# Kernel tuning notes

Hardware: AMD Instinct MI355X
Metric: run time of the kernel (lower is better)

The kernel has to match this reference:

```python
import jax, jax.numpy as jnp
import numpy as np

B, T, C = 4, 2048, 1024
WIN = 16


def setup_inputs() -> dict:
    key = jax.random.key(0)
    ks = jax.random.split(key, 5)
    s = 1.0 / np.sqrt(C)
    return {
        "x": jax.random.normal(ks[0], (B, T, C), dtype=jnp.float32),
        "Wq": jax.random.normal(ks[1], (C, C), dtype=jnp.float32) * s,
        "bq": jnp.zeros((C,), jnp.float32),
        "Wk": jax.random.normal(ks[2], (C, C), dtype=jnp.float32) * s,
        "bk": jnp.zeros((C,), jnp.float32),
        "Wv": jax.random.normal(ks[3], (C, C), dtype=jnp.float32) * s,
        "bv": jnp.zeros((C,), jnp.float32),
        "Wo": jax.random.normal(ks[4], (C, C), dtype=jnp.float32) * s,
        "bo": jnp.zeros((C,), jnp.float32),
        "window": WIN,
    }


def reference(x, Wq, bq, Wk, bk, Wv, bv, Wo, bo, window):
    Bn, Tn, Cn = x.shape
    half = window // 2
    W = 2 * half + 1  # keys per query (window [t-half, t+half])
    q = x @ Wq.T + bq
    k = x @ Wk.T + bk
    v = x @ Wv.T + bv
    offs = jnp.arange(-half, half + 1)              # [W]
    tpos = jnp.arange(Tn)                            # [T]
    idx = tpos[:, None] + offs[None, :]              # [T, W]
    valid = (idx >= 0) & (idx < Tn)                  # [T, W]
    idx_c = jnp.clip(idx, 0, Tn - 1)
    k_win = k[:, idx_c, :]                           # [B, T, W, C]
    v_win = v[:, idx_c, :]                           # [B, T, W, C]
    scale = 1.0 / jnp.sqrt(jnp.asarray(Cn, x.dtype))
    scores = jnp.einsum('btc,btwc->btw', q, k_win) * scale
    scores = jnp.where(valid[None, :, :], scores, jnp.finfo(x.dtype).min)
    attn = jax.nn.softmax(scores, axis=-1)           # [B, T, W]
    ctx = jnp.einsum('btw,btwc->btc', attn, v_win)   # [B, T, C]
    return ctx @ Wo.T + bo
```

## Files before the change

kernel.cpp:

```cpp
#include <hip/hip_runtime.h>
#include <cstdint>
#include <cstddef>

#define B_ 4
#define T_ 2048
#define C_ 1024
#define M_ (B_ * T_)
#define HALF_ 8
#define W_ 17
#define QKV_STRIDE 3072
#define NT 32
#define ATOK 16

typedef unsigned short u16;
typedef _Float16 half8 __attribute__((ext_vector_type(8)));
typedef _Float16 half2_t __attribute__((ext_vector_type(2)));
typedef float f32x16 __attribute__((ext_vector_type(16)));
typedef unsigned short ushort8v __attribute__((ext_vector_type(8)));

__device__ __forceinline__ float dot16(half8 a, half8 b, float acc) {
#if __has_builtin(__builtin_amdgcn_fdot2)
    const half2_t* pa = (const half2_t*)&a;
    const half2_t* pb = (const half2_t*)&b;
#pragma unroll
    for (int e = 0; e < 4; ++e) acc = __builtin_amdgcn_fdot2(pa[e], pb[e], acc, false);
#else
#pragma unroll
    for (int e = 0; e < 8; ++e) acc += (float)a[e] * (float)b[e];
#endif
    return acc;
}

__device__ __forceinline__ ushort4 cvt4(float4 v) {
    ushort4 o;
    _Float16 a = (_Float16)v.x; o.x = __builtin_bit_cast(unsigned short, a);
    _Float16 b = (_Float16)v.y; o.y = __builtin_bit_cast(unsigned short, b);
    _Float16 c = (_Float16)v.z; o.z = __builtin_bit_cast(unsigned short, c);
    _Float16 d = (_Float16)v.w; o.w = __builtin_bit_cast(unsigned short, d);
    return o;
}


__global__ void prologue2(const float* __restrict__ x,
                          const float* __restrict__ Wq, const float* __restrict__ Wk,
                          const float* __restrict__ Wv, const float* __restrict__ Wo,
                          const float* __restrict__ bq, const float* __restrict__ bk,
                          const float* __restrict__ bv,
                          u16* __restrict__ xf, u16* __restrict__ wfq,
                          u16* __restrict__ wfo, float* __restrict__ bcat) {
    const int blk = blockIdx.x;
    const int tid = threadIdx.x;
    if (blk >= 3072) {
        int i = (blk - 3072) * 256 + tid;
        const float* src = (i < 1024) ? bq : (i < 2048) ? bk : bv;
        bcat[i] = src[i & 1023];
        return;
    }
    __shared__ ushort8v g16[512];
    const float* src;
    u16* dst;
    size_t chunk_base;
    int kg;
    if (blk < 2048) {
        const int mt = blk >> 3; kg = blk & 7;
        src = x + (size_t)mt * 32 * C_;
        dst = xf; chunk_base = (size_t)mt * 64;
    } else {
        const int w = blk - 2048;
        const int mat = w >> 8, nt = (w >> 3) & 31; kg = w & 7;
        src = ((mat == 0) ? Wq : (mat == 1) ? Wk : (mat == 2) ? Wv : Wo)
              + (size_t)nt * 32 * C_;
        if (mat < 3) { dst = wfq; chunk_base = (size_t)(mat * 32 + nt) * 64; }
        else         { dst = wfo; chunk_base = (size_t)nt * 64; }
    }
    const int r = tid >> 3, gc = (tid & 7) * 2;
    const float4* s4 = (const float4*)(src + (size_t)r * C_ + kg * 128 + (tid & 7) * 16);
    float4 f0 = s4[0], f1 = s4[1], f2 = s4[2], f3 = s4[3];
    ushort4 h0 = cvt4(f0), h1 = cvt4(f1), h2 = cvt4(f2), h3 = cvt4(f3);
    ushort8v ga, gb;
    ga[0]=h0.x; ga[1]=h0.y; ga[2]=h0.z; ga[3]=h0.w;
    ga[4]=h1.x; ga[5]=h1.y; ga[6]=h1.z; ga[7]=h1.w;
    gb[0]=h2.x; gb[1]=h2.y; gb[2]=h2.z; gb[3]=h2.w;
    gb[4]=h3.x; gb[5]=h3.y; gb[6]=h3.z; gb[7]=h3.w;
    g16[r * 16 + ((gc    ) ^ (r & 15))] = ga;
    g16[r * 16 + ((gc + 1) ^ (r & 15))] = gb;
    __syncthreads();
    const int lane = tid & 63, rr = lane & 31, hi = lane >> 5;
#pragma unroll
    for (int r2 = 0; r2 < 2; ++r2) {
        const int ksl = r2 * 4 + (tid >> 6);
        const int g = ksl * 2 + hi;
        ushort8v v = g16[rr * 16 + (g ^ (rr & 15))];
        *(ushort8v*)(dst + ((chunk_base + kg * 8 + ksl) * 64 + lane) * 8) = v;
    }
}


#define AS1_ __attribute__((address_space(1)))
#define AS3_ __attribute__((address_space(3)))

__device__ __forceinline__ void gload16(const u16* g, u16* l) {
    __builtin_amdgcn_global_load_lds((AS1_ void*)g, (AS3_ void*)l, 16, 0, 0);
}

#define MFMA_ __builtin_amdgcn_mfma_f32_32x32x16_f16

#define STAGE(NB, KT) { const size_t ko = (size_t)(KT) * 1024;            \
    gload16(gA0 + ko, (NB) + lA0); gload16(gA1 + ko, (NB) + lA1);         \
    gload16(gA2 + ko, (NB) + lA2); gload16(gA3 + ko, (NB) + lA3);         \
    gload16(gB0 + ko, (NB) + lB0); gload16(gB1 + ko, (NB) + lB1); }

#define TILE(CB, NB, KT, DOSTG, VW)                                        \
  {                                                                        \
    half8 a0 = *(const half8*)((CB) + oA);                                 \
    half8 a1 = *(const half8*)((CB) + oA + 1024);                          \
    half8 a2 = *(const half8*)((CB) + oA + 2048);                          \
    half8 a3 = *(const half8*)((CB) + oA + 3072);                          \
    half8 b0v = *(const half8*)((CB) + oB);                                \
    half8 b1v = *(const half8*)((CB) + oB + 1024);                         \
    if (DOSTG) STAGE(NB, (KT) + 2);                                        \
    __builtin_amdgcn_s_setprio(1);                                         \
    acc00 = MFMA_(a0, b0v, acc00, 0, 0, 0);                                \
    acc01 = MFMA_(a0, b1v, acc01, 0, 0, 0);                                \
    acc10 = MFMA_(a1, b0v, acc10, 0, 0, 0);                                \
    acc11 = MFMA_(a1, b1v, acc11, 0, 0, 0);                                \
    acc20 = MFMA_(a2, b0v, acc20, 0, 0, 0);                                \
    acc21 = MFMA_(a2, b1v, acc21, 0, 0, 0);                                \
    acc30 = MFMA_(a3, b0v, acc30, 0, 0, 0);                                \
    acc31 = MFMA_(a3, b1v, acc31, 0, 0, 0);                                \
    __builtin_amdgcn_s_setprio(0);                                         \
    a0 = *(const half8*)((CB) + oA + 512);                                 \
    a1 = *(const half8*)((CB) + oA + 1536);                                \
    a2 = *(const half8*)((CB) + oA + 2560);                                \
    a3 = *(const half8*)((CB) + oA + 3584);                                \
    b0v = *(const half8*)((CB) + oB + 512);                                \
    b1v = *(const half8*)((CB) + oB + 1536);                               \
    __builtin_amdgcn_s_setprio(1);                                         \
    acc00 = MFMA_(a0, b0v, acc00, 0, 0, 0);                                \
    acc01 = MFMA_(a0, b1v, acc01, 0, 0, 0);                                \
    acc10 = MFMA_(a1, b0v, acc10, 0, 0, 0);                                \
    acc11 = MFMA_(a1, b1v, acc11, 0, 0, 0);                                \
    acc20 = MFMA_(a2, b0v, acc20, 0, 0, 0);                                \
    acc21 = MFMA_(a2, b1v, acc21, 0, 0, 0);                                \
    acc30 = MFMA_(a3, b0v, acc30, 0, 0, 0);                                \
    acc31 = MFMA_(a3, b1v, acc31, 0, 0, 0);                                \
    __builtin_amdgcn_s_setprio(0);                                         \
    if ((VW) == 6)      asm volatile("s_waitcnt vmcnt(6) lgkmcnt(0)" ::: "memory"); \
    else if ((VW) == 0) asm volatile("s_waitcnt vmcnt(0) lgkmcnt(0)" ::: "memory"); \
    else                asm volatile("s_waitcnt lgkmcnt(0)" ::: "memory"); \
    asm volatile("s_barrier" ::: "memory");                                \
  }

template <int OUT_F16>
__global__ __launch_bounds__(256, 2) void gemm_p2(
    const u16* __restrict__ Afrag, const u16* __restrict__ Bfrag,
    const float* __restrict__ bias, void* __restrict__ Cout, int Ndim)
{
    __shared__ u16 lds[3][12288];
    const int tid  = threadIdx.x;
    const int lane = tid & 63;
    const int wave = tid >> 6;
    const int wm   = wave >> 1;
    const int wn   = wave & 1;
    const int la8  = lane * 8;

    const int nb  = gridDim.x * gridDim.y;
    int bid = blockIdx.y * gridDim.x + blockIdx.x;
    bid = (bid & 7) * (nb >> 3) + (bid >> 3);
    const int bx = bid % gridDim.x;
    const int by = bid / gridDim.x;

    const u16* gA0 = Afrag + ((size_t)(by*8 + ((wave    )>>1))*64 + ((wave    )&1))*512 + la8;
    const u16* gA1 = Afrag + ((size_t)(by*8 + ((wave+ 4 )>>1))*64 + ((wave+ 4 )&1))*512 + la8;
    const u16* gA2 = Afrag + ((size_t)(by*8 + ((wave+ 8 )>>1))*64 + ((wave+ 8 )&1))*512 + la8;
    const u16* gA3 = Afrag + ((size_t)(by*8 + ((wave+12 )>>1))*64 + ((wave+12 )&1))*512 + la8;
    const u16* gB0 = Bfrag + ((size_t)(bx*4 + ((wave    )>>1))*64 + ((wave    )&1))*512 + la8;
    const u16* gB1 = Bfrag + ((size_t)(bx*4 + ((wave+ 4 )>>1))*64 + ((wave+ 4 )&1))*512 + la8;
    const int lA0 = (wave     ) * 512;
    const int lA1 = (wave +  4) * 512;
    const int lA2 = (wave +  8) * 512;
    const int lA3 = (wave + 12) * 512;
    const int lB0 = 8192 + (wave    ) * 512;
    const int lB1 = 8192 + (wave + 4) * 512;

    const int oA = wm * 4096 + la8;
    const int oB = 8192 + wn * 2048 + la8;

    u16* b0 = &lds[0][0];
    u16* b1 = &lds[1][0];
    u16* b2 = &lds[2][0];

    STAGE(b0, 0);
    STAGE(b1, 1);
    asm volatile("s_waitcnt vmcnt(6)" ::: "memory");
    asm volatile("s_barrier" ::: "memory");

    f32x16 acc00, acc01, acc10, acc11, acc20, acc21, acc30, acc31;
#pragma unroll
    for (int r = 0; r < 16; ++r) {
        acc00[r] = 0.f; acc01[r] = 0.f; acc10[r] = 0.f; acc11[r] = 0.f;
        acc20[r] = 0.f; acc21[r] = 0.f; acc30[r] = 0.f; acc31[r] = 0.f;
    }

#pragma unroll 1
    for (int kt = 0; kt < NT - 2; kt += 3) {
        TILE(b0, b2, kt,     1, 6);
        TILE(b1, b0, kt + 1, 1, 6);
        TILE(b2, b1, kt + 2, 1, 6);
    }
    TILE(b0, b2, NT - 2, 0, 0);
    TILE(b1, b2, NT - 1, 0, -1);

    const int m0 = by * 256 + wm * 128;
    const int n0 = bx * 128 + wn * 64;
    f32x16 accs[4][2] = {{acc00, acc01}, {acc10, acc11}, {acc20, acc21}, {acc30, acc31}};
#pragma unroll
    for (int i = 0; i < 4; ++i) {
#pragma unroll
        for (int j = 0; j < 2; ++j) {
            const int col = n0 + j * 32 + (lane & 31);
            const float bv = bias[col];
#pragma unroll
            for (int reg = 0; reg < 16; ++reg) {
                const int row = m0 + i * 32 + (reg & 3) + 8 * (reg >> 2) + 4 * (lane >> 5);
                float val = accs[i][j][reg] + bv;
                if (OUT_F16) {
                    _Float16 h = (_Float16)val;
                    ((u16*)Cout)[(size_t)row * Ndim + col] = __builtin_bit_cast(unsigned short, h);
                } else {
                    ((float*)Cout)[(size_t)row * Ndim + col] = val;
                }
            }
        }
    }
}


#define STAGE_S0(NB, KO) { gload16(gA0 + (KO), (NB) + lsA0); gload16(gB0 + (KO), (NB) + lsB0); }
#define STAGE_S1(NB, KO) { gload16(gA1 + (KO), (NB) + lsA1); gload16(gB1 + (KO), (NB) + lsB1); }

#define TILE_S(CB, NB, KT, DOSTG, VW)                                      \
  {                                                                        \
    const size_t ko = (size_t)((KT) + 2) * 1024;                           \
    half8 a0 = *(const half8*)((CB) + oA);                                 \
    half8 a1 = *(const half8*)((CB) + oA + 1024);                          \
    half8 b0v = *(const half8*)((CB) + oB);                                \
    half8 b1v = *(const half8*)((CB) + oB + 1024);                         \
    if (DOSTG) STAGE_S0(NB, ko);                                           \
    __builtin_amdgcn_s_setprio(1);                                         \
    acc00 = MFMA_(a0, b0v, acc00, 0, 0, 0);                                \
    acc01 = MFMA_(a0, b1v, acc01, 0, 0, 0);                                \
    acc10 = MFMA_(a1, b0v, acc10, 0, 0, 0);                                \
    acc11 = MFMA_(a1, b1v, acc11, 0, 0, 0);                                \
    __builtin_amdgcn_s_setprio(0);                                         \
    a0 = *(const half8*)((CB) + oA + 512);                                 \
    a1 = *(const half8*)((CB) + oA + 1536);                                \
    b0v = *(const half8*)((CB) + oB + 512);                                \
    b1v = *(const half8*)((CB) + oB + 1536);                               \
    if (DOSTG) STAGE_S1(NB, ko);                                           \
    __builtin_amdgcn_s_setprio(1);                                         \
    acc00 = MFMA_(a0, b0v, acc00, 0, 0, 0);                                \
    acc01 = MFMA_(a0, b1v, acc01, 0, 0, 0);                                \
    acc10 = MFMA_(a1, b0v, acc10, 0, 0, 0);                                \
    acc11 = MFMA_(a1, b1v, acc11, 0, 0, 0);                                \
    __builtin_amdgcn_s_setprio(0);                                         \
    if ((VW) == 4)      asm volatile("s_waitcnt vmcnt(4) lgkmcnt(0)" ::: "memory"); \
    else if ((VW) == 0) asm volatile("s_waitcnt vmcnt(0) lgkmcnt(0)" ::: "memory"); \
    else                asm volatile("s_waitcnt lgkmcnt(0)" ::: "memory"); \
    asm volatile("s_barrier" ::: "memory");                                \
  }

__global__ __launch_bounds__(256, 2) void gemm_s(
    const u16* __restrict__ Afrag, const u16* __restrict__ Bfrag,
    const float* __restrict__ bias, float* __restrict__ Cout, int Ndim)
{
    __shared__ u16 lds[3][8192];
    const int tid  = threadIdx.x;
    const int lane = tid & 63;
    const int wave = tid >> 6;
    const int wm   = wave >> 1;
    const int wn   = wave & 1;
    const int la8  = lane * 8;

    const int nb  = gridDim.x * gridDim.y;
    int bid = blockIdx.y * gridDim.x + blockIdx.x;
    bid = (bid & 7) * (nb >> 3) + (bid >> 3);
    const int bx = bid % gridDim.x;
    const int by = bid / gridDim.x;

    const u16* gA0 = Afrag + ((size_t)(by*4 + ((wave    )>>1))*64 + ((wave    )&1))*512 + la8;
    const u16* gA1 = Afrag + ((size_t)(by*4 + ((wave+ 4 )>>1))*64 + ((wave+ 4 )&1))*512 + la8;
    const u16* gB0 = Bfrag + ((size_t)(bx*4 + ((wave    )>>1))*64 + ((wave    )&1))*512 + la8;
    const u16* gB1 = Bfrag + ((size_t)(bx*4 + ((wave+ 4 )>>1))*64 + ((wave+ 4 )&1))*512 + la8;
    const int lsA0 = (wave    ) * 512;
    const int lsA1 = (wave + 4) * 512;
    const int lsB0 = 4096 + (wave    ) * 512;
    const int lsB1 = 4096 + (wave + 4) * 512;

    const int oA = wm * 2048 + la8;
    const int oB = 4096 + wn * 2048 + la8;

    u16* b0 = &lds[0][0];
    u16* b1 = &lds[1][0];
    u16* b2 = &lds[2][0];

    STAGE_S0(b0, 0); STAGE_S1(b0, 0);
    STAGE_S0(b1, 1024); STAGE_S1(b1, 1024);
    asm volatile("s_waitcnt vmcnt(4)" ::: "memory");
    asm volatile("s_barrier" ::: "memory");

    f32x16 acc00, acc01, acc10, acc11;
#pragma unroll
    for (int r = 0; r < 16; ++r) { acc00[r] = 0.f; acc01[r] = 0.f; acc10[r] = 0.f; acc11[r] = 0.f; }

#pragma unroll 1
    for (int kt = 0; kt < NT - 2; kt += 3) {
        TILE_S(b0, b2, kt,     1, 4);
        TILE_S(b1, b0, kt + 1, 1, 4);
        TILE_S(b2, b1, kt + 2, 1, 4);
    }
    TILE_S(b0, b2, NT - 2, 0, 0);
    TILE_S(b1, b2, NT - 1, 0, -1);

    const int m0 = by * 128 + wm * 64;
    const int n0 = bx * 128 + wn * 64;
    f32x16 accs[2][2] = {{acc00, acc01}, {acc10, acc11}};
#pragma unroll
    for (int i = 0; i < 2; ++i) {
#pragma unroll
        for (int j = 0; j < 2; ++j) {
            const int col = n0 + j * 32 + (lane & 31);
            const float bv = bias[col];
#pragma unroll
            for (int reg = 0; reg < 16; ++reg) {
                const int row = m0 + i * 32 + (reg & 3) + 8 * (reg >> 2) + 4 * (lane >> 5);
                Cout[(size_t)row * Ndim + col] = accs[i][j][reg] + bv;
            }
        }
    }
}

__global__ __launch_bounds__(512) void attn_lds(
    const u16* __restrict__ qkv, u16* __restrict__ ctxf)
{
    __shared__ u16 kv[64 * 1024];
    const int tid  = threadIdx.x;
    const int lane = tid & 63;
    const int wave = tid >> 6;
    const int blk  = blockIdx.x;
    const int b    = blk >> 7;
    const int t0   = (blk & 127) * ATOK;
    const int base = b * T_;
    const int c0   = lane * 8;

#pragma unroll
    for (int i = 0; i < 16; ++i) {
        const int c    = wave + 8 * i;
        const int m    = c >> 6;
        const int row  = (c >> 1) & 31;
        const int half = c & 1;
        const int p    = t0 - 8 + row;
        if (p >= 0 && p < T_) {
            gload16(qkv + (size_t)(base + p) * QKV_STRIDE + 1024 * (1 + m) + half * 512 + c0,
                    &kv[(m * 32 + row) * 1024 + half * 512]);
        }
    }
    asm volatile("s_waitcnt vmcnt(0)" ::: "memory");
    __syncthreads();

#pragma unroll
    for (int it = 0; it < 2; ++it) {
        const int t  = t0 + wave * 2 + it;
        const int gt = base + t;
        const half8 q0 = *(const half8*)(qkv + (size_t)gt * QKV_STRIDE + c0);
        const half8 q1 = *(const half8*)(qkv + (size_t)gt * QKV_STRIDE + 512 + c0);

        float s[W_];
#pragma unroll
        for (int o = 0; o < W_; ++o) {
            const int j  = t - HALF_ + o;
            const int jc = min(max(j, 0), T_ - 1);
            const int lr = jc - t0 + 8;
            const u16* kp = &kv[lr * 1024 + c0];
            half8 k0 = *(const half8*)kp;
            half8 k1 = *(const half8*)(kp + 512);
            float d = dot16(q1, k1, dot16(q0, k0, 0.f));
#pragma unroll
            for (int off = 32; off > 0; off >>= 1)
                d += __shfl_xor(d, off);
            s[o] = (j == jc) ? d * 0.03125f : -3.0e38f;
        }

        float mx = s[0];
#pragma unroll
        for (int o = 1; o < W_; ++o) mx = fmaxf(mx, s[o]);
        float den = 0.f;
#pragma unroll
        for (int o = 0; o < W_; ++o) den += __expf(s[o] - mx);
        const float inv = 1.f / den;

        float acc0[8], acc1[8];
#pragma unroll
        for (int e = 0; e < 8; ++e) { acc0[e] = 0.f; acc1[e] = 0.f; }
#pragma unroll
        for (int o = 0; o < W_; ++o) {
            const int j  = t - HALF_ + o;
            const int jc = min(max(j, 0), T_ - 1);
            const int lr = jc - t0 + 8;
            const float wt = __expf(s[o] - mx) * inv;
            const u16* vp = &kv[(32 + lr) * 1024 + c0];
            half8 v0 = *(const half8*)vp;
            half8 v1 = *(const half8*)(vp + 512);
#pragma unroll
            for (int e = 0; e < 8; ++e) {
                acc0[e] += wt * (float)v0[e];
                acc1[e] += wt * (float)v1[e];
            }
        }

        half8 o0, o1;
#pragma unroll
        for (int e = 0; e < 8; ++e) { o0[e] = (_Float16)acc0[e]; o1[e] = (_Float16)acc1[e]; }

        const int m = gt;
        const int mt = m >> 5;
        const int rowin = (m & 31) + 32 * (lane & 1);
        const size_t ch0 = ((size_t)mt * 64 + (lane >> 1)) * 64 + rowin;
        const size_t ch1 = ((size_t)mt * 64 + 32 + (lane >> 1)) * 64 + rowin;
        *(half8*)(ctxf + ch0 * 8) = o0;
        *(half8*)(ctxf + ch1 * 8) = o1;
    }
}

extern "C" void kernel_launch(void* const* d_in, const int* in_sizes, int n_in,
                              void* d_out, int out_size, void* d_ws, size_t ws_size,
                              hipStream_t stream) {
    const float* x  = (const float*)d_in[0];
    const float* Wq = (const float*)d_in[1];
    const float* bq = (const float*)d_in[2];
    const float* Wk = (const float*)d_in[3];
    const float* bk = (const float*)d_in[4];
    const float* Wv = (const float*)d_in[5];
    const float* bv = (const float*)d_in[6];
    const float* Wo = (const float*)d_in[7];
    const float* bo = (const float*)d_in[8];
    float* out = (float*)d_out;

    u16* xf   = (u16*)d_ws;
    u16* wfq  = xf   + (size_t)M_ * C_;
    u16* wfo  = wfq  + (size_t)3 * C_ * C_;
    u16* qkvh = wfo  + (size_t)C_ * C_;
    u16* ctxf = qkvh + (size_t)M_ * QKV_STRIDE;
    float* bcat = (float*)(ctxf + (size_t)M_ * C_);

    prologue2<<<3084, 256, 0, stream>>>(x, Wq, Wk, Wv, Wo, bq, bk, bv,
                                        xf, wfq, wfo, bcat);

    dim3 gqkv(QKV_STRIDE / 128, M_ / 256);
    gemm_p2<1><<<gqkv, 256, 0, stream>>>(xf, wfq, bcat, qkvh, QKV_STRIDE);

    attn_lds<<<M_ / ATOK, 512, 0, stream>>>(qkvh, ctxf);

    dim3 go(C_ / 128, M_ / 128);
    gemm_s<<<go, 256, 0, stream>>>(ctxf, wfo, bo, out, C_);
}
```

Measured before the change: 222.5 us.

## Compute windowed attention with MFMA on fragment-layout Q/K/V from QKV GEMM

The QKV GEMM epilogue now writes Q, K and V into separate buffers in MFMA fragment layouts (V transposed) in place of a row-major interleaved buffer. The attention kernel is replaced by a single-wave MFMA version in which each block of 32 queries computes scores against a 64-key band, applies a masked softmax, and multiplies probabilities by V with MFMAs. This swaps scalar dot products and shuffle reductions for matrix instructions, at the cost of computing about 4x more scores than the 17-wide window needs. The epilogue stores become scattered 2-byte writes.

```diff
diff --git a/kernel.cpp b/kernel.cpp
--- a/kernel.cpp
+++ b/kernel.cpp
@@ -8,28 +8,12 @@
 #define M_ (B_ * T_)
 #define HALF_ 8
 #define W_ 17
-#define QKV_STRIDE 3072
 #define NT 32
-#define ATOK 16
 
 typedef unsigned short u16;
 typedef _Float16 half8 __attribute__((ext_vector_type(8)));
-typedef _Float16 half2_t __attribute__((ext_vector_type(2)));
 typedef float f32x16 __attribute__((ext_vector_type(16)));
 typedef unsigned short ushort8v __attribute__((ext_vector_type(8)));
-
-__device__ __forceinline__ float dot16(half8 a, half8 b, float acc) {
-#if __has_builtin(__builtin_amdgcn_fdot2)
-    const half2_t* pa = (const half2_t*)&a;
-    const half2_t* pb = (const half2_t*)&b;
-#pragma unroll
-    for (int e = 0; e < 4; ++e) acc = __builtin_amdgcn_fdot2(pa[e], pb[e], acc, false);
-#else
-#pragma unroll
-    for (int e = 0; e < 8; ++e) acc += (float)a[e] * (float)b[e];
-#endif
-    return acc;
-}
 
 __device__ __forceinline__ ushort4 cvt4(float4 v) {
     ushort4 o;
@@ -151,10 +135,9 @@
     asm volatile("s_barrier" ::: "memory");                                \
   }
 
-template <int OUT_F16>
-__global__ __launch_bounds__(256, 2) void gemm_p2(
+__global__ __launch_bounds__(256, 2) void gemm_qkv(
     const u16* __restrict__ Afrag, const u16* __restrict__ Bfrag,
-    const float* __restrict__ bias, void* __restrict__ Cout, int Ndim)
+    const float* __restrict__ bias, u16* __restrict__ qkvf)
 {
     __shared__ u16 lds[3][12288];
     const int tid  = threadIdx.x;
@@ -219,22 +202,27 @@
 #pragma unroll
         for (int j = 0; j < 2; ++j) {
             const int col = n0 + j * 32 + (lane & 31);
+            const int mat = col >> 10;
+            const int ch  = col & 1023;
             const float bv = bias[col];
+            u16* dst = qkvf + (size_t)mat * ((size_t)M_ * C_);
 #pragma unroll
             for (int reg = 0; reg < 16; ++reg) {
-                const int row = m0 + i * 32 + (reg & 3) + 8 * (reg >> 2) + 4 * (lane >> 5);
-                float val = accs[i][j][reg] + bv;
-                if (OUT_F16) {
-                    _Float16 h = (_Float16)val;
-                    ((u16*)Cout)[(size_t)row * Ndim + col] = __builtin_bit_cast(unsigned short, h);
+                const int m = m0 + i * 32 + (reg & 3) + 8 * (reg >> 2) + 4 * (lane >> 5);
+                _Float16 h = (_Float16)(accs[i][j][reg] + bv);
+                size_t addr;
+                if (mat < 2) {
+                    addr = (size_t)((m >> 5) * 64 + (ch >> 4)) * 512
+                         + ((m & 31) + 32 * ((ch >> 3) & 1)) * 8 + (ch & 7);
                 } else {
-                    ((float*)Cout)[(size_t)row * Ndim + col] = val;
+                    addr = (size_t)((m >> 4) * 32 + (ch >> 5)) * 512
+                         + ((ch & 31) + 32 * ((m >> 3) & 1)) * 8 + (m & 7);
                 }
+                dst[addr] = __builtin_bit_cast(unsigned short, h);
             }
         }
     }
 }
-
 
 #define STAGE_S0(NB, KO) { gload16(gA0 + (KO), (NB) + lsA0); gload16(gB0 + (KO), (NB) + lsB0); }
 #define STAGE_S1(NB, KO) { gload16(gA1 + (KO), (NB) + lsA1); gload16(gB1 + (KO), (NB) + lsB1); }
@@ -340,95 +328,100 @@
     }
 }
 
-__global__ __launch_bounds__(512) void attn_lds(
-    const u16* __restrict__ qkv, u16* __restrict__ ctxf)
+__global__ __launch_bounds__(64) void attn_mfma(
+    const u16* __restrict__ qf, const u16* __restrict__ kf,
+    const u16* __restrict__ vf, u16* __restrict__ ctxf)
 {
-    __shared__ u16 kv[64 * 1024];
-    const int tid  = threadIdx.x;
-    const int lane = tid & 63;
-    const int wave = tid >> 6;
-    const int blk  = blockIdx.x;
-    const int b    = blk >> 7;
-    const int t0   = (blk & 127) * ATOK;
-    const int base = b * T_;
-    const int c0   = lane * 8;
-
-#pragma unroll
-    for (int i = 0; i < 16; ++i) {
-        const int c    = wave + 8 * i;
-        const int m    = c >> 6;
-        const int row  = (c >> 1) & 31;
-        const int half = c & 1;
-        const int p    = t0 - 8 + row;
-        if (p >= 0 && p < T_) {
-            gload16(qkv + (size_t)(base + p) * QKV_STRIDE + 1024 * (1 + m) + half * 512 + c0,
-                    &kv[(m * 32 + row) * 1024 + half * 512]);
+    const int l   = threadIdx.x;
+    const int q   = l & 31;
+    const int hi  = l >> 5;
+    const int t0  = blockIdx.x * 32;
+    const int t0l = t0 & (T_ - 1);
+
+    const int r1 = min(max(t0 - 16 + q, 0), M_ - 1);
+    const int r2 = min(max(t0 + 16 + q, 0), M_ - 1);
+    const u16* a1p = kf + (size_t)(r1 >> 5) * 32768 + ((r1 & 31) + 32 * hi) * 8;
+    const u16* a2p = kf + (size_t)(r2 >> 5) * 32768 + ((r2 & 31) + 32 * hi) * 8;
+    const u16* qp  = qf + (size_t)(t0 >> 5) * 32768 + l * 8;
+
+    f32x16 sc1, sc2;
+#pragma unroll
+    for (int r = 0; r < 16; ++r) { sc1[r] = 0.f; sc2[r] = 0.f; }
+#pragma unroll 8
+    for (int ks = 0; ks < 64; ++ks) {
+        half8 a1 = *(const half8*)(a1p + ks * 512);
+        half8 a2 = *(const half8*)(a2p + ks * 512);
+        half8 qb = *(const half8*)(qp  + ks * 512);
+        sc1 = MFMA_(a1, qb, sc1, 0, 0, 0);
+        sc2 = MFMA_(a2, qb, sc2, 0, 0, 0);
+    }
+
+    float px1[16], px2[16];
+#pragma unroll
+    for (int r = 0; r < 16; ++r) {
+        px1[r] = __shfl_xor(sc1[r], 32);
+        px2[r] = __shfl_xor(sc2[r], 32);
+    }
+
+    const int plo = max(q + 8, 16 - t0l);
+    const int phi = min(q + 24, (T_ + 15) - t0l);
+    float s[64];
+#pragma unroll
+    for (int p = 0; p < 64; ++p) {
+        const int row = p & 31;
+        const int h   = (row >> 2) & 1;
+        const int rg  = (row & 3) + 4 * (row >> 3);
+        const float own = (p < 32) ? sc1[rg] : sc2[rg];
+        const float oth = (p < 32) ? px1[rg] : px2[rg];
+        const float v = (h == hi) ? own : oth;
+        s[p] = (p >= plo && p <= phi) ? v * 0.03125f : -3.0e38f;
+    }
+
+    float mx = s[0];
+#pragma unroll
+    for (int p = 1; p < 64; ++p) mx = fmaxf(mx, s[p]);
+    float den = 0.f;
+#pragma unroll
+    for (int p = 0; p < 64; ++p) { const float w = __expf(s[p] - mx); s[p] = w; den += w; }
+    const float inv = 1.f / den;
+
+    half8 pa0, pa1, pa2, pa3;
+#pragma unroll
+    for (int e = 0; e < 8; ++e) {
+        pa0[e] = (_Float16)((hi ? s[ 8 + e] : s[ 0 + e]) * inv);
+        pa1[e] = (_Float16)((hi ? s[24 + e] : s[16 + e]) * inv);
+        pa2[e] = (_Float16)((hi ? s[40 + e] : s[32 + e]) * inv);
+        pa3[e] = (_Float16)((hi ? s[56 + e] : s[48 + e]) * inv);
+    }
+
+    const int s0i = (t0 - 16) >> 4;
+    const u16* vb0p = vf + (size_t)min(max(s0i    , 0), M_/16 - 1) * 16384 + l * 8;
+    const u16* vb1p = vf + (size_t)min(max(s0i + 1, 0), M_/16 - 1) * 16384 + l * 8;
+    const u16* vb2p = vf + (size_t)min(max(s0i + 2, 0), M_/16 - 1) * 16384 + l * 8;
+    const u16* vb3p = vf + (size_t)min(max(s0i + 3, 0), M_/16 - 1) * 16384 + l * 8;
+    const size_t ctxb = (size_t)(t0 >> 5) * 32768;
+    const int lpo = 32 * ((l >> 3) & 1);
+    const int e7  = l & 7;
+#pragma unroll 2
+    for (int n = 0; n < 32; ++n) {
+        half8 v0 = *(const half8*)(vb0p + n * 512);
+        half8 v1 = *(const half8*)(vb1p + n * 512);
+        half8 v2 = *(const half8*)(vb2p + n * 512);
+        half8 v3 = *(const half8*)(vb3p + n * 512);
+        f32x16 o;
+#pragma unroll
+        for (int r = 0; r < 16; ++r) o[r] = 0.f;
+        o = MFMA_(pa0, v0, o, 0, 0, 0);
+        o = MFMA_(pa1, v1, o, 0, 0, 0);
+        o = MFMA_(pa2, v2, o, 0, 0, 0);
+        o = MFMA_(pa3, v3, o, 0, 0, 0);
+        u16* cp = ctxf + ctxb + (size_t)(2 * n + (q >> 4)) * 512 + e7;
+#pragma unroll
+        for (int r = 0; r < 16; ++r) {
+            const int mrow = (r & 3) + 8 * (r >> 2) + 4 * hi;
+            _Float16 hv = (_Float16)o[r];
+            cp[(mrow + lpo) * 8] = __builtin_bit_cast(unsigned short, hv);
         }
-    }
-    asm volatile("s_waitcnt vmcnt(0)" ::: "memory");
-    __syncthreads();
-
-#pragma unroll
-    for (int it = 0; it < 2; ++it) {
-        const int t  = t0 + wave * 2 + it;
-        const int gt = base + t;
-        const half8 q0 = *(const half8*)(qkv + (size_t)gt * QKV_STRIDE + c0);
-        const half8 q1 = *(const half8*)(qkv + (size_t)gt * QKV_STRIDE + 512 + c0);
-
-        float s[W_];
-#pragma unroll
-        for (int o = 0; o < W_; ++o) {
-            const int j  = t - HALF_ + o;
-            const int jc = min(max(j, 0), T_ - 1);
-            const int lr = jc - t0 + 8;
-            const u16* kp = &kv[lr * 1024 + c0];
-            half8 k0 = *(const half8*)kp;
-            half8 k1 = *(const half8*)(kp + 512);
-            float d = dot16(q1, k1, dot16(q0, k0, 0.f));
-#pragma unroll
-            for (int off = 32; off > 0; off >>= 1)
-                d += __shfl_xor(d, off);
-            s[o] = (j == jc) ? d * 0.03125f : -3.0e38f;
-        }
-
-        float mx = s[0];
-#pragma unroll
-        for (int o = 1; o < W_; ++o) mx = fmaxf(mx, s[o]);
-        float den = 0.f;
-#pragma unroll
-        for (int o = 0; o < W_; ++o) den += __expf(s[o] - mx);
-        const float inv = 1.f / den;
-
-        float acc0[8], acc1[8];
-#pragma unroll
-        for (int e = 0; e < 8; ++e) { acc0[e] = 0.f; acc1[e] = 0.f; }
-#pragma unroll
-        for (int o = 0; o < W_; ++o) {
-            const int j  = t - HALF_ + o;
-            const int jc = min(max(j, 0), T_ - 1);
-            const int lr = jc - t0 + 8;
-            const float wt = __expf(s[o] - mx) * inv;
-            const u16* vp = &kv[(32 + lr) * 1024 + c0];
-            half8 v0 = *(const half8*)vp;
-            half8 v1 = *(const half8*)(vp + 512);
-#pragma unroll
-            for (int e = 0; e < 8; ++e) {
-                acc0[e] += wt * (float)v0[e];
-                acc1[e] += wt * (float)v1[e];
-            }
-        }
-
-        half8 o0, o1;
-#pragma unroll
-        for (int e = 0; e < 8; ++e) { o0[e] = (_Float16)acc0[e]; o1[e] = (_Float16)acc1[e]; }
-
-        const int m = gt;
-        const int mt = m >> 5;
-        const int rowin = (m & 31) + 32 * (lane & 1);
-        const size_t ch0 = ((size_t)mt * 64 + (lane >> 1)) * 64 + rowin;
-        const size_t ch1 = ((size_t)mt * 64 + 32 + (lane >> 1)) * 64 + rowin;
-        *(half8*)(ctxf + ch0 * 8) = o0;
-        *(half8*)(ctxf + ch1 * 8) = o1;
     }
 }
 
@@ -446,20 +439,21 @@
     const float* bo = (const float*)d_in[8];
     float* out = (float*)d_out;
 
+    const size_t MC = (size_t)M_ * C_;
     u16* xf   = (u16*)d_ws;
-    u16* wfq  = xf   + (size_t)M_ * C_;
-    u16* wfo  = wfq  + (size_t)3 * C_ * C_;
-    u16* qkvh = wfo  + (size_t)C_ * C_;
-    u16* ctxf = qkvh + (size_t)M_ * QKV_STRIDE;
-    float* bcat = (float*)(ctxf + (size_t)M_ * C_);
+    u16* wfq  = xf   + MC;
+    u16* wfo  = wfq  + 3 * (size_t)C_ * C_;
+    u16* qkvf = wfo  + (size_t)C_ * C_;
+    u16* ctxf = qkvf + 3 * MC;
+    float* bcat = (float*)(ctxf + MC);
 
     prologue2<<<3084, 256, 0, stream>>>(x, Wq, Wk, Wv, Wo, bq, bk, bv,
                                         xf, wfq, wfo, bcat);
 
-    dim3 gqkv(QKV_STRIDE / 128, M_ / 256);
-    gemm_p2<1><<<gqkv, 256, 0, stream>>>(xf, wfq, bcat, qkvh, QKV_STRIDE);
-
-    attn_lds<<<M_ / ATOK, 512, 0, stream>>>(qkvh, ctxf);
+    dim3 gqkv(3072 / 128, M_ / 256);
+    gemm_qkv<<<gqkv, 256, 0, stream>>>(xf, wfq, bcat, qkvf);
+
+    attn_mfma<<<M_ / 32, 64, 0, stream>>>(qkvf, qkvf + MC, qkvf + 2 * MC, ctxf);
 
     dim3 go(C_ / 128, M_ / 128);
     gemm_s<<<go, 256, 0, stream>>>(ctxf, wfo, bo, out, C_);
```

Result: slower. 253.1 us (+13.8%).
